# Performance work log

Hardware: AMD Instinct MI355X
Metric: run time of the kernel (lower is better)

The kernel has to match this reference:

```python
import jax, jax.numpy as jnp
import numpy as np

NUM_BINS = 32


def setup_inputs() -> dict:
    key = jax.random.key(0)
    k1, k2, k3 = jax.random.split(key, 3)
    shape = (16, 3, 512, 512)  # NCHW images in [0,1)
    pred = jax.random.uniform(k1, shape, dtype=jnp.float32)
    target = jax.random.uniform(k2, shape, dtype=jnp.float32)
    input_img = jax.random.uniform(k3, shape, dtype=jnp.float32)
    return {"pred": pred, "target": target, "input_img": input_img}


def _binned_means(values, seg_ids, num_segments):
    # per-(channel,bin) masked mean; empty bins -> 0.0 (matches torch branch)
    sums = jax.ops.segment_sum(values, seg_ids, num_segments=num_segments)
    counts = jax.ops.segment_sum(jnp.ones_like(values), seg_ids, num_segments=num_segments)
    return jnp.where(counts > 0, sums / jnp.maximum(counts, 1.0), 0.0)


def reference(pred, target, input_img):
    nb = NUM_BINS
    edges = jnp.linspace(0.0, 1.0, nb + 1)

    # [3, N] per-channel flattened views (channel-major)
    x = jnp.transpose(input_img, (1, 0, 2, 3)).reshape(3, -1)
    p = jnp.transpose(pred, (1, 0, 2, 3)).reshape(-1)
    t = jnp.transpose(target, (1, 0, 2, 3)).reshape(-1)

    # bin i covers [edges[i], edges[i+1]) -> searchsorted(side='right') - 1
    idx = jnp.searchsorted(edges, x, side="right") - 1  # [3, N]
    valid = (idx >= 0) & (idx < nb)  # x == 1.0 or x < 0 falls in no bin
    # fold channel into segment id; invalid ids are out-of-range and dropped
    seg = jnp.where(valid, idx + jnp.arange(3)[:, None] * nb, 3 * nb).reshape(-1)

    pred_curve = _binned_means(p, seg, 3 * nb)    # [3*nb]
    target_curve = _binned_means(t, seg, 3 * nb)  # [3*nb]

    # sum_c l1(pred_curve_c, target_curve_c) / 3 == mean over all 3*nb entries
    return jnp.mean(jnp.abs(pred_curve - target_curve))
```

## Files before the change

kernel.cpp:

```cpp
#include <hip/hip_runtime.h>

#define NB     32
#define NSEG   96
#define TPB    256
#define NROW   128
#define PAD    33
#define F4PT   8
#define NCOPY  32

#define POISON8 0xAAAAAAAAAAAAAAAAull
#define POISON4 0xAAAAAAAAu

typedef float f4 __attribute__((ext_vector_type(4)));

union __align__(16) SMem {
    unsigned int hist[NROW * PAD];
    double       red[128];
};

__global__ __launch_bounds__(TPB, 4) void ccl_fused(
    const f4* __restrict__ pred,
    const f4* __restrict__ target,
    const f4* __restrict__ img,
    long n4,
    unsigned long long* __restrict__ gdiff,
    unsigned int* __restrict__ gcnt,
    unsigned int* __restrict__ done,
    float* __restrict__ out)
{
    __shared__ SMem sm;
    __shared__ int lastflag;

    const int tid = threadIdx.x;
    const long base = (long)blockIdx.x * (TPB * F4PT);
    const int  c    = (int)((base >> 16) % 3);
    unsigned int* h = &sm.hist[(tid >> 1) * PAD];

    f4 xv[F4PT], pv[F4PT], tv[F4PT];
    const bool full = (base + (long)TPB * F4PT) <= n4;

    if (full) {
#pragma unroll
        for (int q = 0; q < F4PT; ++q) {
            long i = base + (long)q * TPB + tid;
            xv[q] = __builtin_nontemporal_load(&img[i]);
            pv[q] = __builtin_nontemporal_load(&pred[i]);
            tv[q] = __builtin_nontemporal_load(&target[i]);
        }
        __builtin_amdgcn_sched_barrier(0);
        {
            uint4* hz = (uint4*)sm.hist;
#pragma unroll
            for (int i = tid; i < (NROW * PAD) / 4; i += TPB)
                hz[i] = (uint4){0u, 0u, 0u, 0u};
        }
        __syncthreads();
#pragma unroll
        for (int q = 0; q < F4PT; ++q) {
            float xs[4] = {xv[q].x, xv[q].y, xv[q].z, xv[q].w};
            float ps[4] = {pv[q].x, pv[q].y, pv[q].z, pv[q].w};
            float ts[4] = {tv[q].x, tv[q].y, tv[q].z, tv[q].w};
#pragma unroll
            for (int e = 0; e < 4; ++e) {
                float xe = xs[e];
                if (xe >= 0.0f && xe < 1.0f) {
                    int b = (int)(xe * 32.0f);
                    float d = ps[e] - ts[e];
                    unsigned pack = (unsigned)fmaf(d, 65536.0f, 131072.5f) + (1u << 24);
                    atomicAdd(&h[b], pack);
                }
            }
        }
    } else {
        {
            uint4* hz = (uint4*)sm.hist;
#pragma unroll
            for (int i = tid; i < (NROW * PAD) / 4; i += TPB)
                hz[i] = (uint4){0u, 0u, 0u, 0u};
        }
        __syncthreads();
#pragma unroll
        for (int q = 0; q < F4PT; ++q) {
            long i = base + (long)q * TPB + tid;
            if (i >= n4) continue;
            f4 xq = __builtin_nontemporal_load(&img[i]);
            f4 pq = __builtin_nontemporal_load(&pred[i]);
            f4 tq = __builtin_nontemporal_load(&target[i]);
            float xs[4] = {xq.x, xq.y, xq.z, xq.w};
            float ps[4] = {pq.x, pq.y, pq.z, pq.w};
            float ts[4] = {tq.x, tq.y, tq.z, tq.w};
#pragma unroll
            for (int e = 0; e < 4; ++e) {
                float xe = xs[e];
                if (xe >= 0.0f && xe < 1.0f) {
                    int b = (int)(xe * 32.0f);
                    float d = ps[e] - ts[e];
                    unsigned pack = (unsigned)fmaf(d, 65536.0f, 131072.5f) + (1u << 24);
                    atomicAdd(&h[b], pack);
                }
            }
        }
    }
    __syncthreads();

    unsigned fx = 0u, cn = 0u;
    {
        int b = tid & 31, g = tid >> 5;
#pragma unroll
        for (int k = 0; k < 16; ++k) {
            unsigned v = sm.hist[(g * 16 + k) * PAD + b];
            cn += v >> 24;
            fx += v & 0xFFFFFFu;
        }
    }
    __syncthreads();
    sm.hist[tid]       = fx;
    sm.hist[TPB + tid] = cn;
    __syncthreads();

    if (tid < 32) {
        unsigned fxt = 0u, cnt = 0u;
#pragma unroll
        for (int k = 0; k < 8; ++k) {
            fxt += sm.hist[tid + 32 * k];
            cnt += sm.hist[TPB + tid + 32 * k];
        }
        if (cnt > 0u) {
            int s = (int)(fxt - (cnt << 17));
            int cp = (int)(blockIdx.x & (NCOPY - 1));
            atomicAdd(&gdiff[cp * NSEG + c * NB + tid], (unsigned long long)(long long)s);
            atomicAdd(&gcnt [cp * NSEG + c * NB + tid], cnt);
        }
    }

    asm volatile("s_waitcnt vmcnt(0)" ::: "memory");
    __syncthreads();
    if (tid == 0) {
        unsigned old = __hip_atomic_fetch_add(done, 1u, __ATOMIC_RELAXED,
                                              __HIP_MEMORY_SCOPE_AGENT);
        lastflag = (old == POISON4 + (unsigned)gridDim.x - 1u);
    }
    __syncthreads();
    if (!lastflag) return;

    double v = 0.0;
    if (tid < NSEG) {
        unsigned long long ds = 0ull;
        unsigned int       ct = 0u;
#pragma unroll
        for (int k = 0; k < NCOPY; ++k) {
            ds += __hip_atomic_load(&gdiff[k * NSEG + tid], __ATOMIC_RELAXED, __HIP_MEMORY_SCOPE_AGENT);
            ct += __hip_atomic_load(&gcnt [k * NSEG + tid], __ATOMIC_RELAXED, __HIP_MEMORY_SCOPE_AGENT);
        }
        ds -= (unsigned long long)NCOPY * POISON8;
        ct -= (unsigned)NCOPY * POISON4;
        if (ct > 0u) {
            double dt = (double)(long long)ds * (1.0 / 65536.0);
            v = fabs(dt / (double)ct);
        }
    }
    if (tid < 128) sm.red[tid] = v;
    __syncthreads();
    for (int off = 64; off > 0; off >>= 1) {
        if (tid < off) sm.red[tid] += sm.red[tid + off];
        __syncthreads();
    }
    if (tid == 0) out[0] = (float)(sm.red[0] / (double)NSEG);
}

extern "C" void kernel_launch(void* const* d_in, const int* in_sizes, int n_in,
                              void* d_out, int out_size, void* d_ws, size_t ws_size,
                              hipStream_t stream) {
    const f4* pred   = (const f4*)d_in[0];
    const f4* target = (const f4*)d_in[1];
    const f4* img    = (const f4*)d_in[2];
    long n4 = (long)in_sizes[0] / 4;

    unsigned long long* gdiff = (unsigned long long*)d_ws;
    unsigned int*       gcnt  = (unsigned int*)((char*)d_ws + (size_t)NCOPY * NSEG * sizeof(unsigned long long));
    unsigned int*       done  = (unsigned int*)((char*)d_ws + (size_t)NCOPY * NSEG * (sizeof(unsigned long long) + sizeof(unsigned int)));


    int nblocks = (int)((n4 + (long)TPB * F4PT - 1) / ((long)TPB * F4PT));
    ccl_fused<<<dim3(nblocks), dim3(TPB), 0, stream>>>(pred, target, img, n4,
                                                       gdiff, gcnt, done, (float*)d_out);
}
```

Measured before the change: 156.0 us.

## Process two tiles per block and give each thread a private LDS histogram row

The grid is halved to 768 blocks when there are exactly 1536 tiles, and each block loops over two tiles spaced a whole grid-stride apart. That stride keeps the channel index unchanged, so block setup, histogram zeroing, the reduction and the global atomics are paid once per two tiles. The histogram grows from 128 to 256 rows so each thread owns a row, which removes LDS atomic contention between thread pairs. The costs are that the second tile's loads are issued only after the first tile is processed, so they are not overlapped, and the larger LDS footprint may lower occupancy.

```diff
diff --git a/kernel.cpp b/kernel.cpp
--- a/kernel.cpp
+++ b/kernel.cpp
@@ -3,7 +3,7 @@
 #define NB     32
 #define NSEG   96
 #define TPB    256
-#define NROW   128
+#define NROW   256
 #define PAD    33
 #define F4PT   8
 #define NCOPY  32
@@ -23,6 +23,8 @@
     const f4* __restrict__ target,
     const f4* __restrict__ img,
     long n4,
+    int  tiles_pb,
+    long stride4,
     unsigned long long* __restrict__ gdiff,
     unsigned int* __restrict__ gcnt,
     unsigned int* __restrict__ done,
@@ -32,71 +34,79 @@
     __shared__ int lastflag;
 
     const int tid = threadIdx.x;
-    const long base = (long)blockIdx.x * (TPB * F4PT);
-    const int  c    = (int)((base >> 16) % 3);
-    unsigned int* h = &sm.hist[(tid >> 1) * PAD];
+    const long base0 = (long)blockIdx.x * (TPB * F4PT);
+    const int  c = (int)((base0 >> 16) % 3);
+    unsigned int* h = &sm.hist[tid * PAD];
 
     f4 xv[F4PT], pv[F4PT], tv[F4PT];
-    const bool full = (base + (long)TPB * F4PT) <= n4;
-
-    if (full) {
+
+    const bool full0 = (base0 + (long)TPB * F4PT) <= n4;
+    if (full0) {
 #pragma unroll
         for (int q = 0; q < F4PT; ++q) {
-            long i = base + (long)q * TPB + tid;
+            long i = base0 + (long)q * TPB + tid;
             xv[q] = __builtin_nontemporal_load(&img[i]);
             pv[q] = __builtin_nontemporal_load(&pred[i]);
             tv[q] = __builtin_nontemporal_load(&target[i]);
         }
-        __builtin_amdgcn_sched_barrier(0);
-        {
-            uint4* hz = (uint4*)sm.hist;
-#pragma unroll
-            for (int i = tid; i < (NROW * PAD) / 4; i += TPB)
-                hz[i] = (uint4){0u, 0u, 0u, 0u};
-        }
-        __syncthreads();
-#pragma unroll
-        for (int q = 0; q < F4PT; ++q) {
-            float xs[4] = {xv[q].x, xv[q].y, xv[q].z, xv[q].w};
-            float ps[4] = {pv[q].x, pv[q].y, pv[q].z, pv[q].w};
-            float ts[4] = {tv[q].x, tv[q].y, tv[q].z, tv[q].w};
-#pragma unroll
-            for (int e = 0; e < 4; ++e) {
-                float xe = xs[e];
-                if (xe >= 0.0f && xe < 1.0f) {
-                    int b = (int)(xe * 32.0f);
-                    float d = ps[e] - ts[e];
-                    unsigned pack = (unsigned)fmaf(d, 65536.0f, 131072.5f) + (1u << 24);
-                    atomicAdd(&h[b], pack);
+    }
+    __builtin_amdgcn_sched_barrier(0);
+    {
+        uint4* hz = (uint4*)sm.hist;
+        for (int i = tid; i < (NROW * PAD) / 4; i += TPB)
+            hz[i] = (uint4){0u, 0u, 0u, 0u};
+    }
+    __syncthreads();
+
+    for (int t = 0; t < tiles_pb; ++t) {
+        const long base = base0 + (long)t * stride4;
+        const bool full = (base + (long)TPB * F4PT) <= n4;
+        if (t > 0 && full) {
+#pragma unroll
+            for (int q = 0; q < F4PT; ++q) {
+                long i = base + (long)q * TPB + tid;
+                xv[q] = __builtin_nontemporal_load(&img[i]);
+                pv[q] = __builtin_nontemporal_load(&pred[i]);
+                tv[q] = __builtin_nontemporal_load(&target[i]);
+            }
+        }
+        if (full) {
+#pragma unroll
+            for (int q = 0; q < F4PT; ++q) {
+                float xs[4] = {xv[q].x, xv[q].y, xv[q].z, xv[q].w};
+                float ps[4] = {pv[q].x, pv[q].y, pv[q].z, pv[q].w};
+                float ts[4] = {tv[q].x, tv[q].y, tv[q].z, tv[q].w};
+#pragma unroll
+                for (int e = 0; e < 4; ++e) {
+                    float xe = xs[e];
+                    if (xe >= 0.0f && xe < 1.0f) {
+                        int b = (int)(xe * 32.0f);
+                        float d = ps[e] - ts[e];
+                        unsigned pack = (unsigned)fmaf(d, 65536.0f, 131072.5f) + (1u << 24);
+                        atomicAdd(&h[b], pack);
+                    }
                 }
             }
-        }
-    } else {
-        {
-            uint4* hz = (uint4*)sm.hist;
-#pragma unroll
-            for (int i = tid; i < (NROW * PAD) / 4; i += TPB)
-                hz[i] = (uint4){0u, 0u, 0u, 0u};
-        }
-        __syncthreads();
-#pragma unroll
-        for (int q = 0; q < F4PT; ++q) {
-            long i = base + (long)q * TPB + tid;
-            if (i >= n4) continue;
-            f4 xq = __builtin_nontemporal_load(&img[i]);
-            f4 pq = __builtin_nontemporal_load(&pred[i]);
-            f4 tq = __builtin_nontemporal_load(&target[i]);
-            float xs[4] = {xq.x, xq.y, xq.z, xq.w};
-            float ps[4] = {pq.x, pq.y, pq.z, pq.w};
-            float ts[4] = {tq.x, tq.y, tq.z, tq.w};
-#pragma unroll
-            for (int e = 0; e < 4; ++e) {
-                float xe = xs[e];
-                if (xe >= 0.0f && xe < 1.0f) {
-                    int b = (int)(xe * 32.0f);
-                    float d = ps[e] - ts[e];
-                    unsigned pack = (unsigned)fmaf(d, 65536.0f, 131072.5f) + (1u << 24);
-                    atomicAdd(&h[b], pack);
+        } else if (base < n4) {
+#pragma unroll
+            for (int q = 0; q < F4PT; ++q) {
+                long i = base + (long)q * TPB + tid;
+                if (i >= n4) continue;
+                f4 xq = __builtin_nontemporal_load(&img[i]);
+                f4 pq = __builtin_nontemporal_load(&pred[i]);
+                f4 tq = __builtin_nontemporal_load(&target[i]);
+                float xs[4] = {xq.x, xq.y, xq.z, xq.w};
+                float ps[4] = {pq.x, pq.y, pq.z, pq.w};
+                float ts[4] = {tq.x, tq.y, tq.z, tq.w};
+#pragma unroll
+                for (int e = 0; e < 4; ++e) {
+                    float xe = xs[e];
+                    if (xe >= 0.0f && xe < 1.0f) {
+                        int b = (int)(xe * 32.0f);
+                        float d = ps[e] - ts[e];
+                        unsigned pack = (unsigned)fmaf(d, 65536.0f, 131072.5f) + (1u << 24);
+                        atomicAdd(&h[b], pack);
+                    }
                 }
             }
         }
@@ -107,8 +117,8 @@
     {
         int b = tid & 31, g = tid >> 5;
 #pragma unroll
-        for (int k = 0; k < 16; ++k) {
-            unsigned v = sm.hist[(g * 16 + k) * PAD + b];
+        for (int k = 0; k < 32; ++k) {
+            unsigned v = sm.hist[(g * 32 + k) * PAD + b];
             cn += v >> 24;
             fx += v & 0xFFFFFFu;
         }
@@ -181,7 +191,16 @@
     unsigned int*       done  = (unsigned int*)((char*)d_ws + (size_t)NCOPY * NSEG * (sizeof(unsigned long long) + sizeof(unsigned int)));
 
 
-    int nblocks = (int)((n4 + (long)TPB * F4PT - 1) / ((long)TPB * F4PT));
-    ccl_fused<<<dim3(nblocks), dim3(TPB), 0, stream>>>(pred, target, img, n4,
-                                                       gdiff, gcnt, done, (float*)d_out);
+    long ntile = (n4 + (long)TPB * F4PT - 1) / ((long)TPB * F4PT);
+    int  grid, tiles_pb;
+    if (ntile == 1536) {
+        grid = 768; tiles_pb = 2;
+    } else {
+        grid = (int)ntile; tiles_pb = 1;
+    }
+    long stride4 = (long)grid * (TPB * F4PT);
+
+    ccl_fused<<<dim3(grid), dim3(TPB), 0, stream>>>(pred, target, img, n4,
+                                                    tiles_pb, stride4,
+                                                    gdiff, gcnt, done, (float*)d_out);
 }
```

Result: faster. 151.3 us (-3.0%).
